# Kernel tuning notes

Measured on AMD Instinct MI355X. Metric: run time of the kernel, lower is better.

Reference implementation:

```python
import jax, jax.numpy as jnp
import numpy as np

STATE_DIM = 5
HIDDEN = 32
B, S = 128, 4096
D_IN = STATE_DIM + 1 + 3  # [h_prev, temp_seq, direction]


def setup_inputs() -> dict:
    key = jax.random.key(0)
    ks = jax.random.split(key, 16)
    g = lambda k, shp: (jax.random.normal(k, shp, dtype=jnp.float32) * 0.1)
    z = lambda shp: jnp.zeros(shp, jnp.float32)
    inp = {}
    inp["h_prev"] = jax.random.normal(ks[0], (B, S, STATE_DIM), dtype=jnp.float32)
    inp["delta_x"] = jax.random.uniform(ks[1], (B, S, 6), dtype=jnp.float32)
    # internal layer 0 (input D_IN -> HIDDEN), layer 1 (HIDDEN -> HIDDEN)
    inp["Wa0"] = g(ks[2], (D_IN, HIDDEN)); inp["ba0"] = z((HIDDEN,))
    inp["Wb0"] = g(ks[3], (D_IN, HIDDEN)); inp["bb0"] = z((HIDDEN,))
    inp["Wa1"] = g(ks[4], (HIDDEN, HIDDEN)); inp["ba1"] = z((HIDDEN,))
    inp["Wb1"] = g(ks[5], (HIDDEN, HIDDEN)); inp["bb1"] = z((HIDDEN,))
    inp["W_alpha"] = g(ks[6], (HIDDEN, 1)); inp["b_alpha"] = z((1,))
    inp["W_beta"]  = g(ks[7], (HIDDEN, 1)); inp["b_beta"]  = z((1,))
    inp["W_gamma"] = g(ks[8], (HIDDEN, 1)); inp["b_gamma"] = z((1,))
    inp["W_c"] = g(ks[9], (HIDDEN, STATE_DIM)); inp["b_c"] = z((STATE_DIM,))
    inp["W_out"] = g(ks[10], (STATE_DIM, 1))  # no bias
    return inp


def reference(h_prev, delta_x, Wa0, ba0, Wb0, bb0, Wa1, ba1, Wb1, bb1,
              W_alpha, b_alpha, W_beta, b_beta, W_gamma, b_gamma,
              W_c, b_c, W_out):
    # delta_x: [delta_strain, delta_time, delta_temp, init_strain, init_time, init_temp]
    df = delta_x[..., :3]                       # (B, S, 3)
    init_temp = delta_x[:, 0:1, 5:6]            # (B, 1, 1) init temp at t=0
    temp_seq = jnp.cumsum(delta_x[..., 2:3], axis=1) + init_temp  # (B, S, 1)
    # normalized increment direction
    norm = jnp.maximum(jnp.sqrt(jnp.sum(df * df, axis=-1, keepdims=True)), 1e-7)
    direction = df / norm                       # (B, S, 3)
    l = jnp.concatenate([h_prev, temp_seq, direction], axis=-1)   # (B, S, 9)
    # two internal tanh*tanh gated dense layers
    l = jnp.tanh(l @ Wa0 + ba0) * jnp.tanh(l @ Wb0 + bb0)         # (B, S, 32)
    l = jnp.tanh(l @ Wa1 + ba1) * jnp.tanh(l @ Wb1 + bb1)         # (B, S, 32)
    # exp gates (non-negative rate params)
    alpha = jnp.exp(l @ W_alpha + b_alpha)      # (B, S, 1)
    beta  = jnp.exp(l @ W_beta  + b_beta)
    gamma = jnp.exp(l @ W_gamma + b_gamma)
    c_n = jnp.tanh(l @ W_c + b_c)               # (B, S, 5)
    # update gate from physical increments
    z = 1.0 - jnp.exp(-alpha * jnp.abs(df[..., 0:1])
                      - beta * df[..., 1:2]
                      - gamma * jnp.abs(df[..., 2:3]))
    h_n = (1.0 - z) * h_prev + z * c_n          # (B, S, 5)
    sigma_n = h_n @ W_out                       # (B, S, 1)
    return (h_n, sigma_n)
```

## Files before the change

### kernel.cpp

```cpp
#include <hip/hip_runtime.h>

#define B_DIMC   128
#define S_DIMC   4096
#define N_TOK    (B_DIMC * S_DIMC)
#define CHUNK    256
#define N_CHUNK  (N_TOK / CHUNK)
#define CPB      (S_DIMC / CHUNK)

typedef __attribute__((ext_vector_type(8))) short  short8;
typedef __attribute__((ext_vector_type(4))) float  floatx4;
typedef __attribute__((ext_vector_type(4))) int    intx4;

__device__ float g_chunksums[N_CHUNK];

__device__ __forceinline__ int cvtpk(float a, float b) {
    int r;
    asm("v_cvt_pk_bf16_f32 %0, %1, %2" : "=v"(r) : "v"(a), "v"(b));
    return r;
}
__device__ __forceinline__ short bf1(float a) { return (short)cvtpk(a, a); }

__device__ __forceinline__ float fast_tanh(float x) {
    float e = __builtin_amdgcn_exp2f(2.885390082f * __builtin_amdgcn_fmed3f(x, -9.0f, 9.0f));
    return fmaf(-2.0f, __builtin_amdgcn_rcpf(e + 1.0f), 1.0f);
}
__device__ __forceinline__ float gate2(float a, float b) {
    const float c = 2.885390082f;
    float ea = __builtin_amdgcn_exp2f(c * __builtin_amdgcn_fmed3f(a, -9.0f, 9.0f));
    float eb = __builtin_amdgcn_exp2f(c * __builtin_amdgcn_fmed3f(b, -9.0f, 9.0f));
    float t  = fmaf(ea, eb, 1.0f);
    float u  = ea + eb;
    return (t - u) * __builtin_amdgcn_rcpf(t + u);
}

__global__ __launch_bounds__(256) void chunksum_kernel(const float* __restrict__ dx) {
    const int lane = threadIdx.x & 63;
    const int wid  = threadIdx.x >> 6;
    __shared__ float wsum[4];
    const float* base = dx + (size_t)blockIdx.x * (CHUNK * 6);
    float s = 0.0f;
    #pragma unroll
    for (int j = threadIdx.x; j < 384; j += 256) {
        const float4 v = *(const float4*)(base + j * 4);
        const int r = j % 3;
        if (r == 0) s += v.z;
        if (r == 2) s += v.x;
    }
    #pragma unroll
    for (int off = 32; off >= 1; off >>= 1) s += __shfl_down(s, off, 64);
    if (lane == 0) wsum[wid] = s;
    __syncthreads();
    if (threadIdx.x == 0)
        g_chunksums[blockIdx.x] = wsum[0] + wsum[1] + wsum[2] + wsum[3];
}

__device__ __forceinline__ float head_w(int n, int k,
                                        const float* Wal, const float* Wbe,
                                        const float* Wga, const float* Wc) {
    if (n == 0) return Wal[k];
    if (n == 1) return Wbe[k];
    if (n == 2) return Wga[k];
    if (n < 8)  return Wc[k * 5 + (n - 3)];
    return 0.0f;
}

union SMemU {
    struct {
        short W[4][32][40];
        short Wh[16][40];
        float Bias[16];
        float Wsum[4];
    } b;
    short A[4][64][40];
};

__global__ __launch_bounds__(256) void msc_kernel(
    const float* __restrict__ h_prev, const float* __restrict__ dx,
    const float* __restrict__ Wa0, const float* __restrict__ ba0,
    const float* __restrict__ Wb0, const float* __restrict__ bb0,
    const float* __restrict__ Wa1, const float* __restrict__ ba1,
    const float* __restrict__ Wb1, const float* __restrict__ bb1,
    const float* __restrict__ W_alpha, const float* __restrict__ b_alpha,
    const float* __restrict__ W_beta,  const float* __restrict__ b_beta,
    const float* __restrict__ W_gamma, const float* __restrict__ b_gamma,
    const float* __restrict__ W_c,     const float* __restrict__ b_c,
    const float* __restrict__ W_out,
    float* __restrict__ out)
{
    __shared__ __align__(16) SMemU sm;

    const int tid  = threadIdx.x;
    const int w    = tid >> 6;
    const int lane = tid & 63;
    const int n    = lane & 15;
    const int quad = lane >> 4;
    const int t    = blockIdx.x * CHUNK + tid;

    const float* hp = h_prev + (size_t)t * 5;
    const float* d  = dx     + (size_t)t * 6;
    const float hp0 = hp[0], hp1 = hp[1], hp2 = hp[2], hp3 = hp[3], hp4 = hp[4];
    const float df0 = d[0], df1 = d[1], df2 = d[2];

    const int batch = blockIdx.x / CPB;
    const int cib   = blockIdx.x % CPB;
    float cs = (lane < cib) ? g_chunksums[batch * CPB + lane] : 0.0f;
    cs += __shfl_xor(cs, 1, 64);
    cs += __shfl_xor(cs, 2, 64);
    cs += __shfl_xor(cs, 4, 64);
    cs += __shfl_xor(cs, 8, 64);
    const float csum = __builtin_bit_cast(float,
        __builtin_amdgcn_readfirstlane(__builtin_bit_cast(int, cs)));
    const float coff = dx[(size_t)batch * S_DIMC * 6 + 5] + csum;

    float w5a[2], w5b[2], bA0[2], bB0[2], bA1[2], bB1[2];
    #pragma unroll
    for (int nt = 0; nt < 2; ++nt) {
        const int col = nt * 16 + n;
        w5a[nt] = Wa0[5 * 32 + col];  w5b[nt] = Wb0[5 * 32 + col];
        bA0[nt] = ba0[col];           bB0[nt] = bb0[col];
        bA1[nt] = ba1[col];           bB1[nt] = bb1[col];
    }

    float x = df2;
    #pragma unroll
    for (int off = 1; off < 64; off <<= 1) {
        float y = __shfl_up(x, off, 64);
        if (lane >= off) x += y;
    }
    if (lane == 63) sm.b.Wsum[w] = x;

    #pragma unroll
    for (int m = 0; m < 4; ++m) {
        const float* Wsrc = (m == 0) ? Wa0 : (m == 1) ? Wb0 : (m == 2) ? Wa1 : Wb1;
        const bool l0 = (m < 2);
        #pragma unroll
        for (int dd = tid; dd < 512; dd += 256) {
            const int col = dd >> 4, kd = dd & 15, k0 = kd * 2, k1 = k0 + 1;
            float v0, v1;
            if (l0) {
                v0 = (k0 < 9 && k0 != 5) ? Wsrc[k0 * 32 + col] : 0.0f;
                v1 = (k1 < 9 && k1 != 5) ? Wsrc[k1 * 32 + col] : 0.0f;
            } else {
                v0 = Wsrc[k0 * 32 + col];
                v1 = Wsrc[k1 * 32 + col];
            }
            ((int*)&sm.b.W[m][col][0])[kd] = cvtpk(v0, v1);
        }
    }
    {
        const int hn = tid >> 4, kd = tid & 15, k0 = kd * 2;
        const float v0 = head_w(hn, k0,     W_alpha, W_beta, W_gamma, W_c);
        const float v1 = head_w(hn, k0 + 1, W_alpha, W_beta, W_gamma, W_c);
        ((int*)&sm.b.Wh[hn][0])[kd] = cvtpk(v0, v1);
    }
    if (tid < 16) {
        sm.b.Bias[tid] = (tid == 0) ? b_alpha[0] : (tid == 1) ? b_beta[0]
                       : (tid == 2) ? b_gamma[0] : (tid < 8) ? b_c[tid - 3] : 0.0f;
    }

    __syncthreads();

    short8 Ba0f[2], Bb0f[2], Ba1f[2], Bb1f[2], Bhf;
    #pragma unroll
    for (int nt = 0; nt < 2; ++nt) {
        const int col = nt * 16 + n;
        Ba0f[nt] = *(const short8*)&sm.b.W[0][col][quad * 8];
        Bb0f[nt] = *(const short8*)&sm.b.W[1][col][quad * 8];
        Ba1f[nt] = *(const short8*)&sm.b.W[2][col][quad * 8];
        Bb1f[nt] = *(const short8*)&sm.b.W[3][col][quad * 8];
    }
    Bhf = *(const short8*)&sm.b.Wh[n][quad * 8];
    const float hbias = sm.b.Bias[n];

    float pre = coff;
    if (w > 0) pre += sm.b.Wsum[0];
    if (w > 1) pre += sm.b.Wsum[1];
    if (w > 2) pre += sm.b.Wsum[2];
    const float temp_t = pre + x;

    __syncthreads();

    const float nrm = fmaxf(sqrtf(df0*df0 + df1*df1 + df2*df2), 1e-7f);
    const float inv = __builtin_amdgcn_rcpf(nrm);
    {
        int* arow = (int*)&sm.A[w][lane][0];
        intx4 v0 = { cvtpk(hp0, hp1), cvtpk(hp2, hp3),
                     cvtpk(hp4, 0.0f), cvtpk(df0*inv, df1*inv) };
        intx4 v1 = { cvtpk(df2*inv, 0.0f), 0, 0, 0 };
        intx4 z4 = { 0, 0, 0, 0 };
        *(intx4*)&arow[0]  = v0;
        *(intx4*)&arow[4]  = v1;
        *(intx4*)&arow[8]  = z4;
        *(intx4*)&arow[12] = z4;
        *(float*)&arow[16] = temp_t;
    }

    #pragma unroll
    for (int mt = 0; mt < 4; ++mt) {
        const short8 Af = *(const short8*)&sm.A[w][mt * 16 + n][quad * 8];
        const int rb = mt * 16 + quad * 4;
        floatx4 tv;
        #pragma unroll
        for (int r = 0; r < 4; ++r)
            tv[r] = *(const float*)&sm.A[w][rb + r][32];
        #pragma unroll
        for (int nt = 0; nt < 2; ++nt) {
            floatx4 Ca, Cb;
            #pragma unroll
            for (int r = 0; r < 4; ++r) {
                Ca[r] = fmaf(tv[r], w5a[nt], bA0[nt]);
                Cb[r] = fmaf(tv[r], w5b[nt], bB0[nt]);
            }
            Ca = __builtin_amdgcn_mfma_f32_16x16x32_bf16(Af, Ba0f[nt], Ca, 0, 0, 0);
            Cb = __builtin_amdgcn_mfma_f32_16x16x32_bf16(Af, Bb0f[nt], Cb, 0, 0, 0);
            #pragma unroll
            for (int r = 0; r < 4; ++r)
                sm.A[w][mt * 16 + quad * 4 + r][nt * 16 + n] = bf1(gate2(Ca[r], Cb[r]));
        }
    }

    #pragma unroll
    for (int mt = 0; mt < 4; ++mt) {
        const short8 Af = *(const short8*)&sm.A[w][mt * 16 + n][quad * 8];
        #pragma unroll
        for (int nt = 0; nt < 2; ++nt) {
            floatx4 Ca = { bA1[nt], bA1[nt], bA1[nt], bA1[nt] };
            floatx4 Cb = { bB1[nt], bB1[nt], bB1[nt], bB1[nt] };
            Ca = __builtin_amdgcn_mfma_f32_16x16x32_bf16(Af, Ba1f[nt], Ca, 0, 0, 0);
            Cb = __builtin_amdgcn_mfma_f32_16x16x32_bf16(Af, Bb1f[nt], Cb, 0, 0, 0);
            #pragma unroll
            for (int r = 0; r < 4; ++r)
                sm.A[w][mt * 16 + quad * 4 + r][nt * 16 + n] = bf1(gate2(Ca[r], Cb[r]));
        }
    }

    short8 Ah[4];
    #pragma unroll
    for (int mt = 0; mt < 4; ++mt)
        Ah[mt] = *(const short8*)&sm.A[w][mt * 16 + n][quad * 8];
    asm volatile("" ::: "memory");

    float* hc = (float*)&sm.A[w][0][0];
    #pragma unroll
    for (int mt = 0; mt < 4; ++mt) {
        floatx4 C = { hbias, hbias, hbias, hbias };
        C = __builtin_amdgcn_mfma_f32_16x16x32_bf16(Ah[mt], Bhf, C, 0, 0, 0);
        if (n < 8) {
            #pragma unroll
            for (int r = 0; r < 4; ++r)
                hc[(mt * 16 + quad * 4 + r) * 12 + n] = C[r];
        }
    }
    asm volatile("" ::: "memory");

    const floatx4 h0v = *(const floatx4*)&hc[lane * 12];
    const floatx4 h1v = *(const floatx4*)&hc[lane * 12 + 4];

    const float alpha = __expf(h0v[0]);
    const float beta  = __expf(h0v[1]);
    const float gamma = __expf(h0v[2]);
    const float z     = 1.0f - __expf(-(alpha * fabsf(df0) + beta * df1 + gamma * fabsf(df2)));
    const float omz   = 1.0f - z;

    const float c0 = fast_tanh(h0v[3]), c1 = fast_tanh(h1v[0]), c2 = fast_tanh(h1v[1]),
                c3 = fast_tanh(h1v[2]), c4 = fast_tanh(h1v[3]);

    const float hn0 = omz * hp0 + z * c0;
    const float hn1 = omz * hp1 + z * c1;
    const float hn2 = omz * hp2 + z * c2;
    const float hn3 = omz * hp3 + z * c3;
    const float hn4 = omz * hp4 + z * c4;

    float* out_h = out + (size_t)t * 5;
    out_h[0] = hn0; out_h[1] = hn1; out_h[2] = hn2; out_h[3] = hn3; out_h[4] = hn4;
    out[(size_t)N_TOK * 5 + t] =
        hn0 * W_out[0] + hn1 * W_out[1] + hn2 * W_out[2] + hn3 * W_out[3] + hn4 * W_out[4];
}

extern "C" void kernel_launch(void* const* d_in, const int* in_sizes, int n_in,
                              void* d_out, int out_size, void* d_ws, size_t ws_size,
                              hipStream_t stream) {
    const float* h_prev  = (const float*)d_in[0];
    const float* dx      = (const float*)d_in[1];
    const float* Wa0     = (const float*)d_in[2];
    const float* ba0     = (const float*)d_in[3];
    const float* Wb0     = (const float*)d_in[4];
    const float* bb0     = (const float*)d_in[5];
    const float* Wa1     = (const float*)d_in[6];
    const float* ba1     = (const float*)d_in[7];
    const float* Wb1     = (const float*)d_in[8];
    const float* bb1     = (const float*)d_in[9];
    const float* W_alpha = (const float*)d_in[10];
    const float* b_alpha = (const float*)d_in[11];
    const float* W_beta  = (const float*)d_in[12];
    const float* b_beta  = (const float*)d_in[13];
    const float* W_gamma = (const float*)d_in[14];
    const float* b_gamma = (const float*)d_in[15];
    const float* W_c     = (const float*)d_in[16];
    const float* b_c     = (const float*)d_in[17];
    const float* W_out   = (const float*)d_in[18];
    float* out = (float*)d_out;

    chunksum_kernel<<<N_CHUNK, CHUNK, 0, stream>>>(dx);
    msc_kernel<<<N_CHUNK, CHUNK, 0, stream>>>(
        h_prev, dx,
        Wa0, ba0, Wb0, bb0, Wa1, ba1, Wb1, bb1,
        W_alpha, b_alpha, W_beta, b_beta, W_gamma, b_gamma,
        W_c, b_c, W_out, out);
}
```

Baseline: 134.1 us.

## Fuse chunk prefix-sum into main kernel by recomputing per-block prefix from input

Removes the separate chunk-sum kernel and its global scratch array. Each block now sums the delta_temp column over all preceding chunks of its batch row itself, reducing via shuffles and shared memory. This drops a launch and the inter-kernel dependency. In exchange, later blocks do quadratically redundant strided reads of dx.

```diff
diff --git a/kernel.cpp b/kernel.cpp
--- a/kernel.cpp
+++ b/kernel.cpp
@@ -10,8 +10,6 @@
 typedef __attribute__((ext_vector_type(8))) short  short8;
 typedef __attribute__((ext_vector_type(4))) float  floatx4;
 typedef __attribute__((ext_vector_type(4))) int    intx4;
-
-__device__ float g_chunksums[N_CHUNK];
 
 __device__ __forceinline__ int cvtpk(float a, float b) {
     int r;
@@ -31,27 +29,6 @@
     float t  = fmaf(ea, eb, 1.0f);
     float u  = ea + eb;
     return (t - u) * __builtin_amdgcn_rcpf(t + u);
-}
-
-__global__ __launch_bounds__(256) void chunksum_kernel(const float* __restrict__ dx) {
-    const int lane = threadIdx.x & 63;
-    const int wid  = threadIdx.x >> 6;
-    __shared__ float wsum[4];
-    const float* base = dx + (size_t)blockIdx.x * (CHUNK * 6);
-    float s = 0.0f;
-    #pragma unroll
-    for (int j = threadIdx.x; j < 384; j += 256) {
-        const float4 v = *(const float4*)(base + j * 4);
-        const int r = j % 3;
-        if (r == 0) s += v.z;
-        if (r == 2) s += v.x;
-    }
-    #pragma unroll
-    for (int off = 32; off >= 1; off >>= 1) s += __shfl_down(s, off, 64);
-    if (lane == 0) wsum[wid] = s;
-    __syncthreads();
-    if (threadIdx.x == 0)
-        g_chunksums[blockIdx.x] = wsum[0] + wsum[1] + wsum[2] + wsum[3];
 }
 
 __device__ __forceinline__ float head_w(int n, int k,
@@ -70,6 +47,7 @@
         short Wh[16][40];
         float Bias[16];
         float Wsum[4];
+        float Wpre[4];
     } b;
     short A[4][64][40];
 };
@@ -103,14 +81,18 @@
 
     const int batch = blockIdx.x / CPB;
     const int cib   = blockIdx.x % CPB;
-    float cs = (lane < cib) ? g_chunksums[batch * CPB + lane] : 0.0f;
-    cs += __shfl_xor(cs, 1, 64);
-    cs += __shfl_xor(cs, 2, 64);
-    cs += __shfl_xor(cs, 4, 64);
-    cs += __shfl_xor(cs, 8, 64);
-    const float csum = __builtin_bit_cast(float,
-        __builtin_amdgcn_readfirstlane(__builtin_bit_cast(int, cs)));
-    const float coff = dx[(size_t)batch * S_DIMC * 6 + 5] + csum;
+    const float* dxb = dx + (size_t)batch * S_DIMC * 6;
+    const int npre = cib * CHUNK;
+    float ps = 0.0f;
+    for (int s = tid; s < npre; s += 256)
+        ps += dxb[(size_t)s * 6 + 2];
+    ps += __shfl_xor(ps, 1, 64);
+    ps += __shfl_xor(ps, 2, 64);
+    ps += __shfl_xor(ps, 4, 64);
+    ps += __shfl_xor(ps, 8, 64);
+    ps += __shfl_xor(ps, 16, 64);
+    ps += __shfl_xor(ps, 32, 64);
+    if (lane == 0) sm.b.Wpre[w] = ps;
 
     float w5a[2], w5b[2], bA0[2], bB0[2], bA1[2], bB1[2];
     #pragma unroll
@@ -172,6 +154,8 @@
     Bhf = *(const short8*)&sm.b.Wh[n][quad * 8];
     const float hbias = sm.b.Bias[n];
 
+    const float coff = dxb[5]
+        + (sm.b.Wpre[0] + sm.b.Wpre[1] + sm.b.Wpre[2] + sm.b.Wpre[3]);
     float pre = coff;
     if (w > 0) pre += sm.b.Wsum[0];
     if (w > 1) pre += sm.b.Wsum[1];
@@ -301,7 +285,6 @@
     const float* W_out   = (const float*)d_in[18];
     float* out = (float*)d_out;
 
-    chunksum_kernel<<<N_CHUNK, CHUNK, 0, stream>>>(dx);
     msc_kernel<<<N_CHUNK, CHUNK, 0, stream>>>(
         h_prev, dx,
         Wa0, ba0, Wb0, bb0, Wa1, ba1, Wb1, bb1,
```

Measured after the change: 140.2 us. +4.6%, slower.
